# Kernel tuning notes

Measured on AMD Instinct MI355X. Metric: run time of the kernel, lower is better.

The kernel has to match this reference:

```python
import jax, jax.numpy as jnp
import numpy as np

EPS = 1e-6

# SIM(3) layout per lietorch: [tx,ty,tz, qx,qy,qz,qw, s]

def quat_mul(q1, q2):
    x1, y1, z1, w1 = jnp.moveaxis(q1, -1, 0)
    x2, y2, z2, w2 = jnp.moveaxis(q2, -1, 0)
    return jnp.stack([
        w1 * x2 + x1 * w2 + y1 * z2 - z1 * y2,
        w1 * y2 - x1 * z2 + y1 * w2 + z1 * x2,
        w1 * z2 + x1 * y2 - y1 * x2 + z1 * w2,
        w1 * w2 - x1 * x2 - y1 * y2 - z1 * z2,
    ], axis=-1)


def quat_rotate(q, v):
    qv, qw = q[..., :3], q[..., 3:4]
    uv = jnp.cross(qv, v)
    return v + 2.0 * (qw * uv + jnp.cross(qv, uv))


def sim3_inv(T):
    t, q, s = T[..., :3], T[..., 3:7], T[..., 7:8]
    q_inv = q * jnp.array([-1.0, -1.0, -1.0, 1.0], dtype=T.dtype)
    s_inv = 1.0 / s
    t_inv = -s_inv * quat_rotate(q_inv, t)
    return jnp.concatenate([t_inv, q_inv, s_inv], axis=-1)


def sim3_mul(T1, T2):
    t1, q1, s1 = T1[..., :3], T1[..., 3:7], T1[..., 7:8]
    t2, q2, s2 = T2[..., :3], T2[..., 3:7], T2[..., 7:8]
    t = t1 + s1 * quat_rotate(q1, t2)
    return jnp.concatenate([t, quat_mul(q1, q2), s1 * s2], axis=-1)


def skew(v):
    x, y, z = v[..., 0], v[..., 1], v[..., 2]
    O = jnp.zeros_like(x)
    return jnp.stack([
        jnp.stack([O, -z, y], -1),
        jnp.stack([z, O, -x], -1),
        jnp.stack([-y, x, O], -1),
    ], -2)


def sim3_log(T):
    t, q, s = T[..., :3], T[..., 3:7], T[..., 7:8]
    qv, qw = q[..., :3], q[..., 3:4]
    nv = jnp.linalg.norm(qv, axis=-1, keepdims=True)
    theta_r = 2.0 * jnp.arctan2(nv, qw)  # rotation angle
    small_r = nv < EPS
    fac = jnp.where(small_r, 2.0, theta_r / jnp.where(small_r, 1.0, nv))
    phi = fac * qv  # so(3) log
    sigma = jnp.log(s)

    # W = C*I + A*Phi + B*Phi^2 (Sophus/lietorch Sim3 calcW), tau = W^{-1} t
    theta = jnp.linalg.norm(phi, axis=-1, keepdims=True)
    sig_small = jnp.abs(sigma) < EPS
    th_small = theta < EPS
    sg = jnp.where(sig_small, 1.0, sigma)
    th = jnp.where(th_small, 1.0, theta)
    scale = jnp.exp(sigma)
    th2, sg2 = th * th, sg * sg
    C = jnp.where(sig_small, 1.0, (scale - 1.0) / sg)
    # sigma ~ 0 branch
    A_ss = jnp.where(th_small, 0.5, (1.0 - jnp.cos(th)) / th2)
    B_ss = jnp.where(th_small, 1.0 / 6.0, (th - jnp.sin(th)) / (th2 * th))
    # generic branch
    a = scale * jnp.sin(th)
    b = scale * jnp.cos(th)
    c = th2 + sg2
    A_g = (a * sg + (1.0 - b) * th) / (th * c)
    B_g = (C - ((b - 1.0) * sg + a * th) / c) / th2
    # theta ~ 0, sigma not small branch
    A_ts = ((sg - 1.0) * scale + 1.0) / sg2
    B_ts = (scale * (sg2 - 2.0 * sg + 2.0) - 2.0) / (2.0 * sg2 * sg)
    A = jnp.where(sig_small, A_ss, jnp.where(th_small, A_ts, A_g))
    B = jnp.where(sig_small, B_ss, jnp.where(th_small, B_ts, B_g))

    Phi = skew(phi)
    I3 = jnp.eye(3, dtype=T.dtype)
    W = C[..., None] * I3 + A[..., None] * Phi + B[..., None] * (Phi @ Phi)
    tau = jnp.linalg.solve(W, t[..., None])[..., 0]
    return jnp.concatenate([tau, phi, sigma], axis=-1)


def _rand_sim3(key, n):
    k1, k2, k3 = jax.random.split(key, 3)
    t = jax.random.normal(k1, (n, 3), dtype=jnp.float32)
    q = jax.random.normal(k2, (n, 4), dtype=jnp.float32)
    q = q / jnp.linalg.norm(q, axis=-1, keepdims=True)
    q = jnp.where(q[:, 3:4] < 0, -q, q)  # w >= 0
    s = jnp.exp(0.1 * jax.random.normal(k3, (n, 1), dtype=jnp.float32))
    return jnp.concatenate([t, q, s], axis=-1)


N_FRAME = 1_000_000
N_LC = N_FRAME - 1


def setup_inputs() -> dict:
    key = jax.random.key(0)
    ks = jax.random.split(key, 7)
    return {
        "Twc": _rand_sim3(ks[0], N_FRAME),
        "Twc_prior_inv": _rand_sim3(ks[1], N_FRAME - 1),
        "Todom_inv": _rand_sim3(ks[2], N_FRAME - 1),
        "prior_weight": jax.random.uniform(ks[3], (N_FRAME - 1, 7), dtype=jnp.float32),
        "odom_weight": jax.random.uniform(ks[4], (N_FRAME - 1, 7), dtype=jnp.float32),
        "edges": jax.random.randint(ks[5], (N_LC, 2), 0, N_FRAME),
        "T_lc": _rand_sim3(ks[6], N_LC),
    }


def reference(Twc, Twc_prior_inv, Todom_inv, prior_weight, odom_weight, edges, T_lc):
    Ti_inv = sim3_inv(Twc[:-1])
    delta = sim3_mul(Ti_inv, Twc[1:])  # Twc[:-1].Inv() * Twc[1:]
    r_prior = sim3_log(sim3_mul(delta, Twc_prior_inv)) * prior_weight
    # NOTE: source uses self.odom_Twc[1:]; in this module only self.Twc exists,
    # so odom delta uses the same pose chain.
    r_odom = sim3_log(sim3_mul(delta, Todom_inv)) * odom_weight
    residual = r_prior + r_odom
    # loop closures: gather poses by edge indices
    delta_lc = sim3_mul(sim3_inv(Twc[edges[:, 0]]), Twc[edges[:, 1]])
    r_lc = sim3_log(sim3_mul(delta_lc, T_lc))
    return residual + r_lc
```

## Files before the change

### kernel.cpp

```cpp
#include <hip/hip_runtime.h>
#include <math.h>

#define EPSF 1e-6f

struct F3   { float x, y, z; };
struct Quat { float x, y, z, w; };
struct Sim3 { F3 t; Quat q; float s; };

__device__ __forceinline__ float frcp(float x) { return __builtin_amdgcn_rcpf(x); }

__device__ __forceinline__ F3 cross3(F3 a, F3 b) {
    return { a.y*b.z - a.z*b.y, a.z*b.x - a.x*b.z, a.x*b.y - a.y*b.x };
}

__device__ __forceinline__ F3 quat_rotate(Quat q, F3 v) {
    F3 qv { q.x, q.y, q.z };
    F3 uv  = cross3(qv, v);
    F3 cuv = cross3(qv, uv);
    return { v.x + 2.0f*(q.w*uv.x + cuv.x),
             v.y + 2.0f*(q.w*uv.y + cuv.y),
             v.z + 2.0f*(q.w*uv.z + cuv.z) };
}

__device__ __forceinline__ Quat quat_mul(Quat a, Quat b) {
    return {
        a.w*b.x + a.x*b.w + a.y*b.z - a.z*b.y,
        a.w*b.y - a.x*b.z + a.y*b.w + a.z*b.x,
        a.w*b.z + a.x*b.y - a.y*b.x + a.z*b.w,
        a.w*b.w - a.x*b.x - a.y*b.y - a.z*b.z
    };
}

__device__ __forceinline__ Sim3 sim3_inv(Sim3 T) {
    Quat qi { -T.q.x, -T.q.y, -T.q.z, T.q.w };
    float si = frcp(T.s);
    F3 r = quat_rotate(qi, T.t);
    return { { -si*r.x, -si*r.y, -si*r.z }, qi, si };
}

__device__ __forceinline__ Sim3 sim3_mul(Sim3 A, Sim3 B) {
    F3 r = quat_rotate(A.q, B.t);
    return { { A.t.x + A.s*r.x, A.t.y + A.s*r.y, A.t.z + A.s*r.z },
             quat_mul(A.q, B.q), A.s * B.s };
}

__device__ __forceinline__ Sim3 load_sim3(const float* __restrict__ p) {
    float4 a = *reinterpret_cast<const float4*>(p);
    float4 b = *reinterpret_cast<const float4*>(p + 4);
    return { {a.x, a.y, a.z}, {a.w, b.x, b.y, b.z}, b.w };
}

__device__ __forceinline__ float fast_atan2_pos(float y, float x) {
    float ax = fabsf(x);
    float mn = fminf(ax, y), mx = fmaxf(ax, y);
    float t  = mn * frcp(mx);
    float t2 = t * t;
    float p = fmaf(t2, -0.0117212f,  0.05265332f);
    p = fmaf(t2, p, -0.11643287f);
    p = fmaf(t2, p,  0.19354346f);
    p = fmaf(t2, p, -0.33262347f);
    p = fmaf(t2, p,  0.99997726f);
    float r = t * p;
    r = (y > ax)   ? 1.57079632679f - r : r;
    r = (x < 0.0f) ? 3.14159265359f - r : r;
    return r;
}

__device__ __forceinline__ void sim3_log(Sim3 T, float out[7]) {
    float qx = T.q.x, qy = T.q.y, qz = T.q.z, qw = T.q.w;
    float nv2 = fmaf(qx, qx, fmaf(qy, qy, qz*qz));
    float nv  = sqrtf(nv2);
    float theta_r = 2.0f * fast_atan2_pos(nv, qw);
    float fac = (nv < EPSF) ? 2.0f : theta_r * frcp(nv);
    float px = fac*qx, py = fac*qy, pz = fac*qz;
    float sigma = __logf(T.s);
    float theta = sqrtf(fmaf(px, px, fmaf(py, py, pz*pz)));

    bool sig_small = fabsf(sigma) < EPSF;
    bool th_small  = theta < EPSF;
    float sg = sig_small ? 1.0f : sigma;
    float th = th_small  ? 1.0f : theta;
    float scale = __expf(sigma);
    float th2 = th*th, sg2 = sg*sg;
    float rsg  = frcp(sg);
    float rth2 = frcp(th2);
    float C = sig_small ? 1.0f : (scale - 1.0f) * rsg;

    float inv_q = frcp(nv2 + qw*qw);
    float sth = 2.0f * qw * nv * inv_q;
    float cth = (qw*qw - nv2) * inv_q;

    float A_ss = th_small ? 0.5f        : (1.0f - cth) * rth2;
    float B_ss = th_small ? (1.0f/6.0f) : (th - sth) * frcp(th2 * th);
    float a = scale * sth;
    float b = scale * cth;
    float c = th2 + sg2;
    float rc = frcp(c);
    float A_g = fmaf(a, sg, (1.0f - b)*th) * frcp(th * c);
    float B_g = (C - fmaf(b - 1.0f, sg, a*th) * rc) * rth2;
    float rsg2 = rsg * rsg;
    float A_ts = fmaf(sg - 1.0f, scale, 1.0f) * rsg2;
    float B_ts = fmaf(scale, fmaf(sg, sg - 2.0f, 2.0f), -2.0f) * (0.5f * rsg2 * rsg);
    float A = sig_small ? A_ss : (th_small ? A_ts : A_g);
    float B = sig_small ? B_ss : (th_small ? B_ts : B_g);

    float P01 = -pz, P02 =  py;
    float P10 =  pz, P12 = -px;
    float P20 = -py, P21 =  px;
    float Q00 = P01*P10 + P02*P20;
    float Q01 = P02*P21;
    float Q02 = P01*P12;
    float Q10 = P12*P20;
    float Q11 = P10*P01 + P12*P21;
    float Q12 = P10*P02;
    float Q20 = P21*P10;
    float Q21 = P20*P01;
    float Q22 = P20*P02 + P21*P12;

    float W00 = fmaf(B, Q00, C);
    float W01 = fmaf(A, P01, B*Q01);
    float W02 = fmaf(A, P02, B*Q02);
    float W10 = fmaf(A, P10, B*Q10);
    float W11 = fmaf(B, Q11, C);
    float W12 = fmaf(A, P12, B*Q12);
    float W20 = fmaf(A, P20, B*Q20);
    float W21 = fmaf(A, P21, B*Q21);
    float W22 = fmaf(B, Q22, C);

    float c00 = fmaf(W11, W22, -W12*W21);
    float c01 = fmaf(W12, W20, -W10*W22);
    float c02 = fmaf(W10, W21, -W11*W20);
    float det = fmaf(W00, c00, fmaf(W01, c01, W02*c02));
    float idet = frcp(det);
    float m01 = fmaf(W02, W21, -W01*W22);
    float m02 = fmaf(W01, W12, -W02*W11);
    float m11 = fmaf(W00, W22, -W02*W20);
    float m12 = fmaf(W02, W10, -W00*W12);
    float m21 = fmaf(W01, W20, -W00*W21);
    float m22 = fmaf(W00, W11, -W01*W10);
    float tx = T.t.x, ty = T.t.y, tz = T.t.z;
    out[0] = fmaf(c00, tx, fmaf(m01, ty, m02*tz)) * idet;
    out[1] = fmaf(c01, tx, fmaf(m11, ty, m12*tz)) * idet;
    out[2] = fmaf(c02, tx, fmaf(m21, ty, m22*tz)) * idet;
    out[3] = px; out[4] = py; out[5] = pz; out[6] = sigma;
}

__global__ void __launch_bounds__(256) pgo_kernel(
        const float* __restrict__ Twc,
        const float* __restrict__ Tp_inv,
        const float* __restrict__ To_inv,
        const float* __restrict__ pw,
        const float* __restrict__ ow,
        const int*   __restrict__ edges,
        const float* __restrict__ T_lc,
        float*       __restrict__ out,
        int n) {
    int i = blockIdx.x * blockDim.x + threadIdx.x;
    if (i >= n) return;
    size_t i8 = (size_t)i * 8;
    size_t i7 = (size_t)i * 7;

    int2 e = *reinterpret_cast<const int2*>(edges + 2*(size_t)i);
    Sim3 Ta = load_sim3(Twc + (size_t)e.x * 8);
    Sim3 Tb = load_sim3(Twc + (size_t)e.y * 8);
    Sim3 Ti = load_sim3(Twc + i8);
    Sim3 Tj = load_sim3(Twc + i8 + 8);
    Sim3 Tp = load_sim3(Tp_inv + i8);
    Sim3 To = load_sim3(To_inv + i8);
    Sim3 Tl = load_sim3(T_lc + i8);

    Sim3 delta = sim3_mul(sim3_inv(Ti), Tj);

    float rp[7], ro[7], rl[7];
    sim3_log(sim3_mul(delta, Tp), rp);
    sim3_log(sim3_mul(delta, To), ro);
    sim3_log(sim3_mul(sim3_mul(sim3_inv(Ta), Tb), Tl), rl);

    #pragma unroll
    for (int k = 0; k < 7; ++k) {
        out[i7 + k] = fmaf(rp[k], pw[i7 + k], fmaf(ro[k], ow[i7 + k], rl[k]));
    }
}

extern "C" void kernel_launch(void* const* d_in, const int* in_sizes, int n_in,
                              void* d_out, int out_size, void* d_ws, size_t ws_size,
                              hipStream_t stream) {
    const float* Twc   = (const float*)d_in[0];
    const float* Tp    = (const float*)d_in[1];
    const float* To    = (const float*)d_in[2];
    const float* pw    = (const float*)d_in[3];
    const float* ow    = (const float*)d_in[4];
    const int*   edges = (const int*)d_in[5];
    const float* Tlc   = (const float*)d_in[6];
    float* out = (float*)d_out;

    int n = in_sizes[1] / 8;
    const int block = 256;
    int grid = (n + block - 1) / block;
    pgo_kernel<<<grid, block, 0, stream>>>(Twc, Tp, To, pw, ow, edges, Tlc, out, n);
}
```

Measured before the change: 217.9 us.

## Process four elements per thread with double-buffered software-pipelined loads

Each thread now handles four strided elements and prefetches the next element's poses into a second register buffer while computing the current one. Scheduling barriers keep the prefetch and compute phases apart, and streaming inputs use nontemporal loads. The aim is to hide gather and load latency behind the ALU-heavy log computation. In exchange it uses more registers and launches a quarter as many threads, which can lower occupancy.

Measured after the change: 222.4 us. +2.1%, slower.

```diff
diff --git a/kernel.cpp b/kernel.cpp
--- a/kernel.cpp
+++ b/kernel.cpp
@@ -2,6 +2,9 @@
 #include <math.h>
 
 #define EPSF 1e-6f
+
+typedef float  f32x4 __attribute__((ext_vector_type(4)));
+typedef int    i32x2 __attribute__((ext_vector_type(2)));
 
 struct F3   { float x, y, z; };
 struct Quat { float x, y, z, w; };
@@ -45,8 +48,14 @@
 }
 
 __device__ __forceinline__ Sim3 load_sim3(const float* __restrict__ p) {
-    float4 a = *reinterpret_cast<const float4*>(p);
-    float4 b = *reinterpret_cast<const float4*>(p + 4);
+    f32x4 a = *reinterpret_cast<const f32x4*>(p);
+    f32x4 b = *reinterpret_cast<const f32x4*>(p + 4);
+    return { {a.x, a.y, a.z}, {a.w, b.x, b.y, b.z}, b.w };
+}
+
+__device__ __forceinline__ Sim3 load_sim3_nt(const float* __restrict__ p) {
+    f32x4 a = __builtin_nontemporal_load(reinterpret_cast<const f32x4*>(p));
+    f32x4 b = __builtin_nontemporal_load(reinterpret_cast<const f32x4*>(p) + 1);
     return { {a.x, a.y, a.z}, {a.w, b.x, b.y, b.z}, b.w };
 }
 
@@ -145,6 +154,8 @@
     out[3] = px; out[4] = py; out[5] = pz; out[6] = sigma;
 }
 
+#define R 4
+
 __global__ void __launch_bounds__(256) pgo_kernel(
         const float* __restrict__ Twc,
         const float* __restrict__ Tp_inv,
@@ -154,31 +165,69 @@
         const int*   __restrict__ edges,
         const float* __restrict__ T_lc,
         float*       __restrict__ out,
-        int n) {
-    int i = blockIdx.x * blockDim.x + threadIdx.x;
-    if (i >= n) return;
-    size_t i8 = (size_t)i * 8;
-    size_t i7 = (size_t)i * 7;
-
-    int2 e = *reinterpret_cast<const int2*>(edges + 2*(size_t)i);
-    Sim3 Ta = load_sim3(Twc + (size_t)e.x * 8);
-    Sim3 Tb = load_sim3(Twc + (size_t)e.y * 8);
-    Sim3 Ti = load_sim3(Twc + i8);
-    Sim3 Tj = load_sim3(Twc + i8 + 8);
-    Sim3 Tp = load_sim3(Tp_inv + i8);
-    Sim3 To = load_sim3(To_inv + i8);
-    Sim3 Tl = load_sim3(T_lc + i8);
-
-    Sim3 delta = sim3_mul(sim3_inv(Ti), Tj);
-
-    float rp[7], ro[7], rl[7];
-    sim3_log(sim3_mul(delta, Tp), rp);
-    sim3_log(sim3_mul(delta, To), ro);
-    sim3_log(sim3_mul(sim3_mul(sim3_inv(Ta), Tb), Tl), rl);
-
+        int n, int q) {
+    int t = blockIdx.x * blockDim.x + threadIdx.x;
+    if (t >= q) return;
+
+    int   ic[R];
+    bool  val[R];
     #pragma unroll
-    for (int k = 0; k < 7; ++k) {
-        out[i7 + k] = fmaf(rp[k], pw[i7 + k], fmaf(ro[k], ow[i7 + k], rl[k]));
+    for (int k = 0; k < R; ++k) {
+        int idx = t + k * q;
+        val[k] = (idx < n);
+        ic[k]  = val[k] ? idx : 0;
+    }
+
+    i32x2 e[R];
+    #pragma unroll
+    for (int k = 0; k < R; ++k)
+        e[k] = *(reinterpret_cast<const i32x2*>(edges) + ic[k]);
+
+    Sim3 Ta[2], Tb[2], Ti[2], Tj[2], Tp[2], To[2], Tl[2];
+
+    {
+        size_t r8 = (size_t)ic[0] * 8;
+        Ta[0] = load_sim3(Twc + (size_t)e[0].x * 8);
+        Tb[0] = load_sim3(Twc + (size_t)e[0].y * 8);
+        Ti[0] = load_sim3(Twc + r8);
+        Tj[0] = load_sim3(Twc + r8 + 8);
+        Tp[0] = load_sim3_nt(Tp_inv + r8);
+        To[0] = load_sim3_nt(To_inv + r8);
+        Tl[0] = load_sim3_nt(T_lc + r8);
+    }
+
+    #pragma unroll
+    for (int k = 0; k < R; ++k) {
+        const int cur = k & 1, nxt = cur ^ 1;
+
+        if (k + 1 < R) {
+            size_t r8 = (size_t)ic[k+1] * 8;
+            Ta[nxt] = load_sim3(Twc + (size_t)e[k+1].x * 8);
+            Tb[nxt] = load_sim3(Twc + (size_t)e[k+1].y * 8);
+            Ti[nxt] = load_sim3(Twc + r8);
+            Tj[nxt] = load_sim3(Twc + r8 + 8);
+            Tp[nxt] = load_sim3_nt(Tp_inv + r8);
+            To[nxt] = load_sim3_nt(To_inv + r8);
+            Tl[nxt] = load_sim3_nt(T_lc + r8);
+        }
+        __builtin_amdgcn_sched_barrier(0);
+
+        Sim3 delta = sim3_mul(sim3_inv(Ti[cur]), Tj[cur]);
+        float rp[7], ro[7], rl[7];
+        sim3_log(sim3_mul(delta, Tp[cur]), rp);
+        sim3_log(sim3_mul(delta, To[cur]), ro);
+        sim3_log(sim3_mul(sim3_mul(sim3_inv(Ta[cur]), Tb[cur]), Tl[cur]), rl);
+
+        if (val[k]) {
+            size_t i7 = (size_t)ic[k] * 7;
+            #pragma unroll
+            for (int j = 0; j < 7; ++j) {
+                float w1 = __builtin_nontemporal_load(pw + i7 + j);
+                float w2 = __builtin_nontemporal_load(ow + i7 + j);
+                out[i7 + j] = fmaf(rp[j], w1, fmaf(ro[j], w2, rl[j]));
+            }
+        }
+        __builtin_amdgcn_sched_barrier(0);
     }
 }
 
@@ -195,7 +244,8 @@
     float* out = (float*)d_out;
 
     int n = in_sizes[1] / 8;
+    int q = (n + R - 1) / R;
     const int block = 256;
-    int grid = (n + block - 1) / block;
-    pgo_kernel<<<grid, block, 0, stream>>>(Twc, Tp, To, pw, ow, edges, Tlc, out, n);
-}
+    int grid = (q + block - 1) / block;
+    pgo_kernel<<<grid, block, 0, stream>>>(Twc, Tp, To, pw, ow, edges, Tlc, out, n, q);
+}
```
